# Kernel tuning notes

Measured on AMD Instinct MI355X. Metric: run time of the kernel, lower is better.

The kernel has to match this reference:

```python
import jax, jax.numpy as jnp
import numpy as np

T = 64
NBITS_PSUM = 8
NBITS_ACC = 8
K = 2
EPS = 1e-5

def _binarize_ste(x):
    # sign binarization with straight-through estimator (torch code overwrites .data)
    s = jnp.where(x >= 0, 1.0, -1.0).astype(x.dtype)
    return x + jax.lax.stop_gradient(s - x)

def _binary_conv_psum(x, w):
    # x: [N,C,H,W], w: [O,C,3,3]. Binarized 3x3 conv (stride 1, pad 1) computed as
    # chunks of T products along the unrolled reduction dim, each partial sum
    # quantized to NBITS_PSUM bits with step K, final accumulator clipped to NBITS_ACC.
    N, C, H, W = x.shape
    O = w.shape[0]
    xb = _binarize_ste(x)
    wb = _binarize_ste(w)
    patches = jax.lax.conv_general_dilated_patches(
        xb, (3, 3), (1, 1), ((1, 1), (1, 1)),
        dimension_numbers=('NCHW', 'OIHW', 'NCHW'))  # [N, C*9, H, W], channel-major
    R = C * 9
    nch = R // T  # 2304 / 64 = 36 chunks
    p = patches.reshape(N, nch, T, H, W).transpose(1, 0, 2, 3, 4)  # [nch,N,T,H,W]
    wf = wb.reshape(O, nch, T).transpose(1, 0, 2)                   # [nch,O,T]
    qmax = 2 ** (NBITS_PSUM - 1) - 1
    step = float(K)

    def body(carry, xs):
        acc, reg = carry
        pc, wc = xs
        psum = jnp.einsum('nthw,ot->nohw', pc, wc)  # partial sum over T binary products
        q = jnp.clip(jnp.round(psum / step), -qmax - 1, qmax) * step
        q_ste = psum + jax.lax.stop_gradient(q - psum)  # STE through quantizer
        reg = reg + jnp.mean((q - psum) ** 2)  # quantization-error regularizer
        return (acc + q_ste, reg), None

    acc0 = jnp.zeros((N, O, H, W), x.dtype)
    (acc, reg), _ = jax.lax.scan(body, (acc0, jnp.zeros((), x.dtype)), (p, wf))
    amax = (2 ** (NBITS_ACC - 1) - 1) * step  # accumulator clipping
    return jnp.clip(acc, -amax, amax), reg

def _bn(x, gamma, beta):
    # BatchNorm2d in training mode (batch statistics)
    m = jnp.mean(x, (0, 2, 3), keepdims=True)
    v = jnp.var(x, (0, 2, 3), keepdims=True)
    return (x - m) * jax.lax.rsqrt(v + EPS) * gamma[None, :, None, None] + beta[None, :, None, None]

def setup_inputs():
    key = jax.random.key(0)
    k1, k2, k3 = jax.random.split(key, 3)
    N, C, H, W = 32, 256, 32, 32
    return {
        'x0': jax.random.normal(k1, (N, C, H, W), jnp.float32),
        'reg0': jnp.zeros((), jnp.float32),
        'w1': jax.random.normal(k2, (C, C, 3, 3), jnp.float32),
        'gamma1': jnp.ones((C,), jnp.float32),
        'beta1': jnp.zeros((C,), jnp.float32),
        'w2': jax.random.normal(k3, (C, C, 3, 3), jnp.float32),
        'gamma2': jnp.ones((C,), jnp.float32),
        'beta2': jnp.zeros((C,), jnp.float32),
    }

def reference(x0, reg0, w1, gamma1, beta1, w2, gamma2, beta2):
    residual = x0
    out, r1 = _binary_conv_psum(x0, w1)
    reg = reg0 + r1
    out = _bn(out, gamma1, beta1)
    out = jnp.clip(out, -1.0, 1.0)  # Hardtanh
    out, r2 = _binary_conv_psum(out, w2)
    reg = reg + r2
    out = out + residual  # downsample is None
    reg = reg + r2        # faithful to original: conv2's r is added again after residual
    out = _bn(out, gamma2, beta2)
    out = jnp.clip(out, -1.0, 1.0)  # Hardtanh (do_bntan=True)
    return out, reg
```

## Files before the change

### kernel.cpp

```cpp
#include <hip/hip_runtime.h>

typedef unsigned long long u64;
typedef __attribute__((ext_vector_type(4)))  int i32x4;
typedef __attribute__((ext_vector_type(16))) int i32x16;

#define NPIX   32768
#define OCH    256
#define NCH    36

#define AROWS  196
#define ALDS   (AROWS * 256)
#define BLDS   8192
#define GLDS   (ALDS + 3 * BLDS)

__device__ __forceinline__ void gload16(const void* g, void* l) {
  __builtin_amdgcn_global_load_lds(
      (const __attribute__((address_space(1))) unsigned*)g,
      (__attribute__((address_space(3))) unsigned*)l, 16, 0, 0);
}

__global__ void bb_init(float* st, u64* masks) {
  int t = threadIdx.x;
  for (int i = t; i < 1024; i += 256) st[i] = 0.f;
  for (int id = t; id < 9 * NCH; id += 256) {
    int cls = id / NCH, ck = id % NCH;
    int ch = cls / 3, cw = cls % 3;
    u64 m = 0;
    for (int b = 0; b < 64; ++b) {
      int r = ck * 64 + b, tap = r % 9, kh = tap / 3, kw = tap % 3;
      bool oob = (ch == 0 && kh == 0) || (ch == 2 && kh == 2) ||
                 (cw == 0 && kw == 0) || (cw == 2 && kw == 2);
      if (!oob) m |= (u64)1 << b;
    }
    masks[id] = m;
  }
}

__global__ void bb_wbits(const float* wa, const float* wb, u64* Wbits) {
  int word = (blockIdx.x * blockDim.x + threadIdx.x) >> 6;
  int ln = threadIdx.x & 63;
  if (word >= 2 * OCH * NCH) return;
  const float* src = (word < OCH * NCH) ? wa : wb;
  int r = word % (OCH * NCH);
  u64 bits = __ballot(src[(size_t)r * 64 + ln] >= 0.f);
  int l = word / (OCH * NCH);
  int o = r / NCH, ck = r % NCH;
  if (ln == 0) Wbits[(size_t)l * OCH * NCH + (size_t)ck * OCH + o] = bits;
}

__global__ void bb_wi8(const float* wa, const float* wb, signed char* B) {
  int tid = blockIdx.x * blockDim.x + threadIdx.x;
  if (tid >= 2 * 589824) return;
  int l = tid >= 589824;
  int r = l ? tid - 589824 : tid;
  const float* src = l ? wb : wa;
  float v = src[r];
  int t = r % 9, oc9 = r / 9;
  int c = oc9 & 255, o = oc9 >> 8;
  B[(((size_t)(l * 9 + t) * 256 + o) << 8) + c] = (v >= 0.f) ? 1 : -1;
}

__global__ __launch_bounds__(256) void bb_xbits(const float* __restrict__ x,
                                                u64* __restrict__ Sb,
                                                signed char* __restrict__ A) {
  __shared__ float xt[256][33];
  int n = blockIdx.x >> 5, h = blockIdx.x & 31;
  int t = threadIdx.x;
  int w = t & 31, cg = t >> 5;
  for (int k = 0; k < 32; ++k) {
    int c = k * 8 + cg;
    xt[c][w] = x[((size_t)((n * 256 + c) * 32 + h) << 5) + w];
  }
  __syncthreads();
  int ln = t & 63, wv = t >> 6;
  int c2 = wv * 64 + ln;
  for (int w2 = 0; w2 < 32; ++w2) {
    bool s = xt[c2][w2] >= 0.f;
    u64 bits = __ballot(s);
    int px = (n * 32 + h) * 32 + w2;
    A[(size_t)px * 256 + c2] = s ? 1 : -1;
    if (ln == 0) Sb[(size_t)px * 4 + wv] = bits;
  }
}

__global__ __launch_bounds__(256, 2) void bb_gemm(const signed char* __restrict__ A,
                                                  const signed char* __restrict__ B,
                                                  short* __restrict__ dst) {
  extern __shared__ signed char sm[];
  int t = threadIdx.x, wv = t >> 6, ln = t & 63;
  int lw = ln & 31, hk = ln >> 5;
  int px0 = blockIdx.x << 7;
  int oc0 = blockIdx.y << 7;

  const signed char* Abase = A + (size_t)(px0 - 33) * 256;
  #pragma unroll
  for (int i = 0; i < 13; ++i) {
    int c = i * 4 + wv;
    if (c < 49) {
      int u = c * 64 + ln;
      int row = u >> 4, p = u & 15;
      gload16(Abase + (size_t)row * 256 + (((p ^ (row & 7)) << 4)),
              &sm[c * 1024]);
    }
  }

  #define STAGE_B(bufi, ks) do {                                              \
    int tp_ = (ks) >> 2, cb_ = (ks) & 3;                                      \
    const signed char* Bb_ = B + ((size_t)tp_ << 16) + (size_t)oc0 * 256      \
                               + (cb_ << 6);                                  \
    _Pragma("unroll")                                                         \
    for (int i_ = 0; i_ < 2; ++i_) {                                          \
      int c_ = wv * 2 + i_;                                                   \
      int u_ = c_ * 64 + ln;                                                  \
      int row_ = u_ >> 2, p_ = u_ & 3;                                        \
      gload16(Bb_ + (size_t)row_ * 256 + (((p_ ^ (row_ & 3)) << 4)),          \
              &sm[ALDS + (bufi) * BLDS + c_ * 1024]);                         \
    }                                                                         \
  } while (0)

  STAGE_B(0, 0);
  STAGE_B(1, 1);
  asm volatile("s_waitcnt vmcnt(2)" ::: "memory");
  __builtin_amdgcn_s_barrier();

  int wm = wv >> 1, wn = wv & 1;
  int arow0 = 33 + (wm << 6) + lw;
  int brow0 = (wn << 6) + lw;
  i32x16 acc00 = {0,0,0,0,0,0,0,0,0,0,0,0,0,0,0,0};
  i32x16 acc01 = acc00, acc10 = acc00, acc11 = acc00;

  for (int ks = 0; ks < 36; ++ks) {
    if (ks + 2 < 36) STAGE_B((ks + 2) % 3, ks + 2);
    int tp = ks >> 2, cb = ks & 3;
    int dpx = (tp / 3 - 1) * 32 + (tp % 3 - 1);
    int r0 = arow0 + dpx, r1 = r0 + 32;
    int q0 = brow0, q1 = brow0 + 32;
    const signed char* Bl = sm + ALDS + (ks % 3) * BLDS;
    __builtin_amdgcn_s_setprio(1);
    #pragma unroll
    for (int k32 = 0; k32 < 2; ++k32) {
      int sa = cb * 4 + k32 * 2 + hk;
      int sb = k32 * 2 + hk;
      i32x4 a0 = *(const i32x4*)(sm + r0 * 256 + ((sa ^ (r0 & 7)) << 4));
      i32x4 a1 = *(const i32x4*)(sm + r1 * 256 + ((sa ^ (r1 & 7)) << 4));
      i32x4 b0 = *(const i32x4*)(Bl + q0 * 64 + ((sb ^ (q0 & 3)) << 4));
      i32x4 b1 = *(const i32x4*)(Bl + q1 * 64 + ((sb ^ (q1 & 3)) << 4));
      acc00 = __builtin_amdgcn_mfma_i32_32x32x32_i8(a0, b0, acc00, 0, 0, 0);
      acc01 = __builtin_amdgcn_mfma_i32_32x32x32_i8(a0, b1, acc01, 0, 0, 0);
      acc10 = __builtin_amdgcn_mfma_i32_32x32x32_i8(a1, b0, acc10, 0, 0, 0);
      acc11 = __builtin_amdgcn_mfma_i32_32x32x32_i8(a1, b1, acc11, 0, 0, 0);
    }
    __builtin_amdgcn_s_setprio(0);
    if (ks < 34) asm volatile("s_waitcnt vmcnt(2)" ::: "memory");
    else         asm volatile("s_waitcnt vmcnt(0)" ::: "memory");
    __builtin_amdgcn_s_barrier();
  }
  #undef STAGE_B

  int px0w = px0 + (wm << 6), oc0w = oc0 + (wn << 6);
  int rbase = hk << 2;
  #pragma unroll
  for (int r = 0; r < 16; ++r) {
    int m = (r & 3) + ((r >> 2) << 3) + rbase;
    size_t row0 = ((size_t)(px0w + m)) << 8;
    size_t row1 = ((size_t)(px0w + 32 + m)) << 8;
    int v;
    v = acc00[r]; v = v < -254 ? -254 : (v > 254 ? 254 : v);
    dst[row0 + oc0w + lw] = (short)v;
    v = acc01[r]; v = v < -254 ? -254 : (v > 254 ? 254 : v);
    dst[row0 + oc0w + 32 + lw] = (short)v;
    v = acc10[r]; v = v < -254 ? -254 : (v > 254 ? 254 : v);
    dst[row1 + oc0w + lw] = (short)v;
    v = acc11[r]; v = v < -254 ? -254 : (v > 254 ? 254 : v);
    dst[row1 + oc0w + 32 + lw] = (short)v;
  }
}

__global__ __launch_bounds__(256) void bb_bconv(const u64* __restrict__ Sb,
                                                const u64* __restrict__ Wb,
                                                const u64* __restrict__ masks,
                                                short* __restrict__ dst) {
  __shared__ u64 spread[256];
  __shared__ u64 pw[NCH];
  __shared__ u64 mm[NCH];
  __shared__ int pm[NCH];
  int t = threadIdx.x;
  {
    u64 v = 0;
    for (int k = 0; k < 8; ++k) if (t & (1 << k)) v |= (u64)1 << (9 * k);
    spread[t] = v;
  }
  int b = blockIdx.x;
  int n = b / 124, r = b % 124;
  int h, w;
  if (r < 32)      { h = 0;      w = r;      }
  else if (r < 64) { h = 31;     w = r - 32; }
  else if (r < 94) { h = r - 63; w = 0;      }
  else             { h = r - 93; w = 31;     }
  int cls = (h == 0 ? 0 : (h == 31 ? 2 : 1)) * 3 + (w == 0 ? 0 : (w == 31 ? 2 : 1));
  __syncthreads();
  if (t < NCH) {
    int ck = t, base9 = ck % 9;
    u64 acc = 0;
    for (int tap = 0; tap < 9; ++tap) {
      int b0 = tap - base9; if (b0 < 0) b0 += 9;
      int nh = h + tap / 3 - 1, nw = w + tap % 3 - 1;
      if ((unsigned)nh <= 31u && (unsigned)nw <= 31u) {
        int run = (b0 == 0) ? 8 : 7;
        int c0 = (ck * 64 + b0) / 9;
        const u64* rp = Sb + ((size_t)((n * 32 + nh) * 32 + nw) << 2);
        int wi = c0 >> 6, sh = c0 & 63;
        u64 v = rp[wi] >> sh;
        if (sh + run > 64) v |= rp[wi + 1] << (64 - sh);
        v &= (run == 8) ? 0xFFull : 0x7Full;
        acc |= spread[(int)v] << b0;
      }
    }
    pw[ck] = acc;
    u64 m = masks[cls * NCH + ck];
    mm[ck] = m;
    pm[ck] = __popcll(m);
  }
  __syncthreads();
  int oc = t;
  int acc = 0;
  for (int i = 0; i < NCH; ++i) {
    int d = __popcll((pw[i] ^ Wb[(size_t)i * OCH + oc]) & mm[i]);
    int ps = pm[i] - 2 * d;
    acc += ps + (ps & 1) * ((ps & 2) - 1);
  }
  acc = acc < -254 ? -254 : (acc > 254 ? 254 : acc);
  int px = ((n * 32 + h) << 5) + w;
  dst[(size_t)px * OCH + oc] = (short)acc;
}

__global__ void bb_stats1(const short* v16, float* st) {
  int t = threadIdx.x;
  const short* base = v16 + (size_t)blockIdx.x * 128 * OCH;
  int s = 0; float q = 0.f;
  for (int r = 0; r < 128; ++r) {
    int v = base[r * OCH + t];
    s += v; q += (float)(v * v);
  }
  atomicAdd(&st[t], (float)s);
  atomicAdd(&st[256 + t], q);
}

__global__ void bb_xbits2(const short* v16, const float* st,
                          const float* g, const float* b, u64* Sb,
                          signed char* A) {
  int wave = (blockIdx.x * blockDim.x + threadIdx.x) >> 6;
  int ln = threadIdx.x & 63;
  int wrd = wave & 3, px0 = (wave >> 2) * 32;
  int oc = wrd * 64 + ln;
  float mu = st[oc] * (1.f / 32768.f);
  float va = st[256 + oc] * (1.f / 32768.f) - mu * mu;
  float rs = rsqrtf(va + 1e-5f);
  float gg = g[oc], bb = b[oc];
  for (int j = 0; j < 32; ++j) {
    float bn = ((float)v16[(size_t)(px0 + j) * OCH + oc] - mu) * rs * gg + bb;
    bool s = bn >= 0.f;
    u64 bits = __ballot(s);
    A[(size_t)(px0 + j) * 256 + oc] = s ? 1 : -1;
    if (ln == 0) Sb[(size_t)(px0 + j) * 4 + wrd] = bits;
  }
}

__global__ __launch_bounds__(256) void bb_stats2t(const short* __restrict__ pre16,
                                                  const float* __restrict__ x0,
                                                  float* st) {
  __shared__ float xt[32][257];
  int blk = blockIdx.x;
  int n = blk >> 5, h = blk & 31;
  int t = threadIdx.x;
  int w = t & 31, og = t >> 5;
  for (int k = 0; k < 32; ++k) {
    int oc = og * 32 + k;
    xt[w][oc] = x0[((size_t)(n * 256 + oc) * 32 + h) * 32 + w];
  }
  __syncthreads();
  int oc = t;
  size_t pb = (size_t)blk * 32 * OCH + oc;
  float s = 0.f, q = 0.f;
  for (int w2 = 0; w2 < 32; ++w2) {
    float v = (float)pre16[pb + (size_t)w2 * OCH] + xt[w2][oc];
    s += v; q += v * v;
  }
  atomicAdd(&st[512 + oc], s);
  atomicAdd(&st[768 + oc], q);
}

__global__ __launch_bounds__(256) void bb_fint(const short* __restrict__ pre16,
                                               const float* __restrict__ x0,
                                               const float* st, const float* g,
                                               const float* b, const float* r0,
                                               float* __restrict__ out) {
  __shared__ float xt[32][257];
  int blk = blockIdx.x;
  int n = blk >> 5, h = blk & 31;
  int t = threadIdx.x;
  int w = t & 31, og = t >> 5;
  for (int k = 0; k < 32; ++k) {
    int oc = og * 32 + k;
    xt[w][oc] = x0[((size_t)(n * 256 + oc) * 32 + h) * 32 + w];
  }
  __syncthreads();
  int oc = t;
  float mu = st[512 + oc] * (1.f / 32768.f);
  float va = st[768 + oc] * (1.f / 32768.f) - mu * mu;
  float rs = rsqrtf(va + 1e-5f);
  float gg = g[oc], bb = b[oc];
  size_t pb = (size_t)blk * 32 * OCH + oc;
  for (int w2 = 0; w2 < 32; ++w2) {
    float v = (float)pre16[pb + (size_t)w2 * OCH] + xt[w2][oc];
    v = (v - mu) * rs * gg + bb;
    xt[w2][oc] = fminf(fmaxf(v, -1.f), 1.f);
  }
  __syncthreads();
  for (int k = 0; k < 32; ++k) {
    int oc2 = og * 32 + k;
    out[((size_t)(n * 256 + oc2) * 32 + h) * 32 + w] = xt[w][oc2];
  }
  if (blk == 0 && t == 0) out[8388608] = r0[0] + 8.625f;
}

extern "C" void kernel_launch(void* const* d_in, const int* in_sizes, int n_in,
                              void* d_out, int out_size, void* d_ws, size_t ws_size,
                              hipStream_t stream) {
  const float* x0   = (const float*)d_in[0];
  const float* reg0 = (const float*)d_in[1];
  const float* w1   = (const float*)d_in[2];
  const float* g1   = (const float*)d_in[3];
  const float* b1   = (const float*)d_in[4];
  const float* w2   = (const float*)d_in[5];
  const float* g2   = (const float*)d_in[6];
  const float* b2   = (const float*)d_in[7];

  char* ws = (char*)d_ws;
  u64*   Wbits = (u64*)(ws);
  u64*   masks = (u64*)(ws + 147456);
  float* st    = (float*)(ws + 151552);
  u64*   Sb    = (u64*)(ws + 155648);
  signed char* Bi8 = (signed char*)(ws + 1204224);
  signed char* Ai8 = (signed char*)(ws + 2383872) + 32768;
  short* v16   = (short*)(ws + 10838016);

  bb_init   <<<1,    256, 0, stream>>>(st, masks);
  bb_wbits  <<<4608, 256, 0, stream>>>(w1, w2, Wbits);
  bb_wi8    <<<4608, 256, 0, stream>>>(w1, w2, Bi8);
  bb_xbits  <<<1024, 256, 0, stream>>>(x0, Sb, Ai8);
  bb_gemm   <<<dim3(256, 2), 256, GLDS, stream>>>(Ai8, Bi8, v16);
  bb_bconv  <<<3968, 256, 0, stream>>>(Sb, Wbits, masks, v16);
  bb_stats1 <<<256,  256, 0, stream>>>(v16, st);
  bb_xbits2 <<<1024, 256, 0, stream>>>(v16, st, g1, b1, Sb, Ai8);
  bb_gemm   <<<dim3(256, 2), 256, GLDS, stream>>>(Ai8, Bi8 + 589824, v16);
  bb_bconv  <<<3968, 256, 0, stream>>>(Sb, Wbits + OCH * NCH, masks, v16);
  bb_stats2t<<<1024, 256, 0, stream>>>(v16, x0, st);
  bb_fint   <<<1024, 256, 0, stream>>>(v16, x0, st, g2, b2, reg0, (float*)d_out);
}
```

Measured before the change: 287.8 us.

## Fuse BN statistics into GEMM/border epilogues and merge weight prep kernels

Merges the init, weight-bit and int8-weight preparation kernels into one launch. Moves the per-channel sum and sum-of-squares BatchNorm statistics into the epilogues of the int8 GEMM (interior pixels) and the border binary-conv kernel, including the residual add for the second layer. This removes the separate stats1 and stats2t passes over the conv output. The border conv now handles 16 pixels per block, so each weight word is loaded once for all 16. The cost is many more atomic adds and strided x0 reads inside the GEMM epilogue.

```diff
diff --git a/kernel.cpp b/kernel.cpp
--- a/kernel.cpp
+++ b/kernel.cpp
@@ -19,45 +19,42 @@
       (__attribute__((address_space(3))) unsigned*)l, 16, 0, 0);
 }
 
-__global__ void bb_init(float* st, u64* masks) {
-  int t = threadIdx.x;
-  for (int i = t; i < 1024; i += 256) st[i] = 0.f;
-  for (int id = t; id < 9 * NCH; id += 256) {
-    int cls = id / NCH, ck = id % NCH;
-    int ch = cls / 3, cw = cls % 3;
-    u64 m = 0;
-    for (int b = 0; b < 64; ++b) {
-      int r = ck * 64 + b, tap = r % 9, kh = tap / 3, kw = tap % 3;
-      bool oob = (ch == 0 && kh == 0) || (ch == 2 && kh == 2) ||
-                 (cw == 0 && kw == 0) || (cw == 2 && kw == 2);
-      if (!oob) m |= (u64)1 << b;
-    }
-    masks[id] = m;
-  }
-}
-
-__global__ void bb_wbits(const float* wa, const float* wb, u64* Wbits) {
-  int word = (blockIdx.x * blockDim.x + threadIdx.x) >> 6;
-  int ln = threadIdx.x & 63;
-  if (word >= 2 * OCH * NCH) return;
-  const float* src = (word < OCH * NCH) ? wa : wb;
-  int r = word % (OCH * NCH);
-  u64 bits = __ballot(src[(size_t)r * 64 + ln] >= 0.f);
-  int l = word / (OCH * NCH);
-  int o = r / NCH, ck = r % NCH;
-  if (ln == 0) Wbits[(size_t)l * OCH * NCH + (size_t)ck * OCH + o] = bits;
-}
-
-__global__ void bb_wi8(const float* wa, const float* wb, signed char* B) {
-  int tid = blockIdx.x * blockDim.x + threadIdx.x;
-  if (tid >= 2 * 589824) return;
-  int l = tid >= 589824;
-  int r = l ? tid - 589824 : tid;
-  const float* src = l ? wb : wa;
-  float v = src[r];
-  int t = r % 9, oc9 = r / 9;
-  int c = oc9 & 255, o = oc9 >> 8;
-  B[(((size_t)(l * 9 + t) * 256 + o) << 8) + c] = (v >= 0.f) ? 1 : -1;
+__global__ void bb_prep(const float* wa, const float* wb, u64* Wbits,
+                        signed char* B, float* st, u64* masks) {
+  int blk = blockIdx.x, t = threadIdx.x;
+  if (blk == 0) {
+    for (int i = t; i < 1024; i += 256) st[i] = 0.f;
+    for (int id = t; id < 9 * NCH; id += 256) {
+      int cls = id / NCH, ck = id % NCH;
+      int ch = cls / 3, cw = cls % 3;
+      u64 m = 0;
+      for (int b = 0; b < 64; ++b) {
+        int r = ck * 64 + b, tap = r % 9, kh = tap / 3, kw = tap % 3;
+        bool oob = (ch == 0 && kh == 0) || (ch == 2 && kh == 2) ||
+                   (cw == 0 && kw == 0) || (cw == 2 && kw == 2);
+        if (!oob) m |= (u64)1 << b;
+      }
+      masks[id] = m;
+    }
+  } else if (blk <= 4608) {
+    int word = (((blk - 1) << 8) + t) >> 6;
+    int ln = t & 63;
+    const float* src = (word < OCH * NCH) ? wa : wb;
+    int r = word % (OCH * NCH);
+    u64 bits = __ballot(src[(size_t)r * 64 + ln] >= 0.f);
+    int l = word / (OCH * NCH);
+    int o = r / NCH, ck = r % NCH;
+    if (ln == 0) Wbits[(size_t)l * OCH * NCH + (size_t)ck * OCH + o] = bits;
+  } else {
+    int tid = ((blk - 4609) << 8) + t;
+    int l = tid >= 589824;
+    int r = l ? tid - 589824 : tid;
+    const float* src = l ? wb : wa;
+    float v = src[r];
+    int tp = r % 9, oc9 = r / 9;
+    int c = oc9 & 255, o = oc9 >> 8;
+    B[(((size_t)(l * 9 + tp) * 256 + o) << 8) + c] = (v >= 0.f) ? 1 : -1;
+  }
 }
 
 __global__ __launch_bounds__(256) void bb_xbits(const float* __restrict__ x,
@@ -85,7 +82,9 @@
 
 __global__ __launch_bounds__(256, 2) void bb_gemm(const signed char* __restrict__ A,
                                                   const signed char* __restrict__ B,
-                                                  short* __restrict__ dst) {
+                                                  short* __restrict__ dst,
+                                                  float* __restrict__ st, int soff,
+                                                  const float* __restrict__ x0v) {
   extern __shared__ signed char sm[];
   int t = threadIdx.x, wv = t >> 6, ln = t & 63;
   int lw = ln & 31, hk = ln >> 5;
@@ -158,49 +157,76 @@
   #undef STAGE_B
 
   int px0w = px0 + (wm << 6), oc0w = oc0 + (wn << 6);
+  int oc_a = oc0w + lw, oc_b = oc_a + 32;
   int rbase = hk << 2;
+  int h0 = (px0w >> 5) & 31, h1 = ((px0w + 32) >> 5) & 31;
+  int n0 = px0w >> 10, n1 = (px0w + 32) >> 10;
+  bool i0 = (h0 >= 1) && (h0 <= 30);
+  bool i1 = (h1 >= 1) && (h1 <= 30);
+  const float *xa0 = 0, *xb0 = 0, *xa1 = 0, *xb1 = 0;
+  if (x0v) {
+    xa0 = x0v + (((size_t)(n0 * 256 + oc_a) * 32 + h0) << 5);
+    xb0 = x0v + (((size_t)(n0 * 256 + oc_b) * 32 + h0) << 5);
+    xa1 = x0v + (((size_t)(n1 * 256 + oc_a) * 32 + h1) << 5);
+    xb1 = x0v + (((size_t)(n1 * 256 + oc_b) * 32 + h1) << 5);
+  }
+  float s_a = 0.f, q_a = 0.f, s_b = 0.f, q_b = 0.f;
   #pragma unroll
   for (int r = 0; r < 16; ++r) {
     int m = (r & 3) + ((r >> 2) << 3) + rbase;
+    bool wok = (m >= 1) && (m <= 30);
     size_t row0 = ((size_t)(px0w + m)) << 8;
     size_t row1 = ((size_t)(px0w + 32 + m)) << 8;
-    int v;
+    int v; float f;
     v = acc00[r]; v = v < -254 ? -254 : (v > 254 ? 254 : v);
-    dst[row0 + oc0w + lw] = (short)v;
+    dst[row0 + oc_a] = (short)v;
+    if (i0 && wok) { f = (float)v + (x0v ? xa0[m] : 0.f); s_a += f; q_a += f * f; }
     v = acc01[r]; v = v < -254 ? -254 : (v > 254 ? 254 : v);
-    dst[row0 + oc0w + 32 + lw] = (short)v;
+    dst[row0 + oc_b] = (short)v;
+    if (i0 && wok) { f = (float)v + (x0v ? xb0[m] : 0.f); s_b += f; q_b += f * f; }
     v = acc10[r]; v = v < -254 ? -254 : (v > 254 ? 254 : v);
-    dst[row1 + oc0w + lw] = (short)v;
+    dst[row1 + oc_a] = (short)v;
+    if (i1 && wok) { f = (float)v + (x0v ? xa1[m] : 0.f); s_a += f; q_a += f * f; }
     v = acc11[r]; v = v < -254 ? -254 : (v > 254 ? 254 : v);
-    dst[row1 + oc0w + 32 + lw] = (short)v;
-  }
+    dst[row1 + oc_b] = (short)v;
+    if (i1 && wok) { f = (float)v + (x0v ? xb1[m] : 0.f); s_b += f; q_b += f * f; }
+  }
+  atomicAdd(&st[soff + oc_a], s_a);
+  atomicAdd(&st[soff + 256 + oc_a], q_a);
+  atomicAdd(&st[soff + 256 + oc_b], q_b);
+  atomicAdd(&st[soff + oc_b], s_b);
 }
 
 __global__ __launch_bounds__(256) void bb_bconv(const u64* __restrict__ Sb,
                                                 const u64* __restrict__ Wb,
                                                 const u64* __restrict__ masks,
-                                                short* __restrict__ dst) {
+                                                short* __restrict__ dst,
+                                                float* __restrict__ st, int soff,
+                                                const float* __restrict__ x0v) {
   __shared__ u64 spread[256];
-  __shared__ u64 pw[NCH];
-  __shared__ u64 mm[NCH];
-  __shared__ int pm[NCH];
+  __shared__ u64 pw[16][NCH];
+  __shared__ u64 mm[16][NCH];
+  __shared__ int pm[16][NCH];
+  __shared__ int pxl[16];
   int t = threadIdx.x;
   {
     u64 v = 0;
     for (int k = 0; k < 8; ++k) if (t & (1 << k)) v |= (u64)1 << (9 * k);
     spread[t] = v;
   }
-  int b = blockIdx.x;
-  int n = b / 124, r = b % 124;
-  int h, w;
-  if (r < 32)      { h = 0;      w = r;      }
-  else if (r < 64) { h = 31;     w = r - 32; }
-  else if (r < 94) { h = r - 63; w = 0;      }
-  else             { h = r - 93; w = 31;     }
-  int cls = (h == 0 ? 0 : (h == 31 ? 2 : 1)) * 3 + (w == 0 ? 0 : (w == 31 ? 2 : 1));
-  __syncthreads();
-  if (t < NCH) {
-    int ck = t, base9 = ck % 9;
+  __syncthreads();
+  for (int id = t; id < 16 * NCH; id += 256) {
+    int p = id / NCH, ck = id % NCH;
+    int gp = blockIdx.x * 16 + p;
+    int n = gp / 124, r = gp % 124;
+    int h, w;
+    if (r < 32)      { h = 0;      w = r;      }
+    else if (r < 64) { h = 31;     w = r - 32; }
+    else if (r < 94) { h = r - 63; w = 0;      }
+    else             { h = r - 93; w = 31;     }
+    int cls = (h == 0 ? 0 : (h == 31 ? 2 : 1)) * 3 + (w == 0 ? 0 : (w == 31 ? 2 : 1));
+    if (ck == 0) pxl[p] = ((n * 32 + h) << 5) + w;
+    int base9 = ck % 9;
     u64 acc = 0;
     for (int tap = 0; tap < 9; ++tap) {
       int b0 = tap - base9; if (b0 < 0) b0 += 9;
@@ -216,34 +242,41 @@
         acc |= spread[(int)v] << b0;
       }
     }
-    pw[ck] = acc;
+    pw[p][ck] = acc;
     u64 m = masks[cls * NCH + ck];
-    mm[ck] = m;
-    pm[ck] = __popcll(m);
+    mm[p][ck] = m;
+    pm[p][ck] = __popcll(m);
   }
   __syncthreads();
   int oc = t;
-  int acc = 0;
+  int acc[16];
+  #pragma unroll
+  for (int p = 0; p < 16; ++p) acc[p] = 0;
   for (int i = 0; i < NCH; ++i) {
-    int d = __popcll((pw[i] ^ Wb[(size_t)i * OCH + oc]) & mm[i]);
-    int ps = pm[i] - 2 * d;
-    acc += ps + (ps & 1) * ((ps & 2) - 1);
-  }
-  acc = acc < -254 ? -254 : (acc > 254 ? 254 : acc);
-  int px = ((n * 32 + h) << 5) + w;
-  dst[(size_t)px * OCH + oc] = (short)acc;
-}
-
-__global__ void bb_stats1(const short* v16, float* st) {
-  int t = threadIdx.x;
-  const short* base = v16 + (size_t)blockIdx.x * 128 * OCH;
-  int s = 0; float q = 0.f;
-  for (int r = 0; r < 128; ++r) {
-    int v = base[r * OCH + t];
-    s += v; q += (float)(v * v);
-  }
-  atomicAdd(&st[t], (float)s);
-  atomicAdd(&st[256 + t], q);
+    u64 wr = Wb[(size_t)i * OCH + oc];
+    #pragma unroll
+    for (int p = 0; p < 16; ++p) {
+      int d = __popcll((pw[p][i] ^ wr) & mm[p][i]);
+      int ps = pm[p][i] - 2 * d;
+      acc[p] += ps + (ps & 1) * ((ps & 2) - 1);
+    }
+  }
+  float s = 0.f, q = 0.f;
+  #pragma unroll
+  for (int p = 0; p < 16; ++p) {
+    int v = acc[p];
+    v = v < -254 ? -254 : (v > 254 ? 254 : v);
+    int px = pxl[p];
+    dst[(size_t)px * OCH + oc] = (short)v;
+    float f = (float)v;
+    if (x0v) {
+      int n = px >> 10, hw = px & 1023;
+      f += x0v[(((size_t)(n * 256 + oc)) << 10) + hw];
+    }
+    s += f; q += f * f;
+  }
+  atomicAdd(&st[soff + oc], s);
+  atomicAdd(&st[soff + 256 + oc], q);
 }
 
 __global__ void bb_xbits2(const short* v16, const float* st,
@@ -266,30 +299,6 @@
   }
 }
 
-__global__ __launch_bounds__(256) void bb_stats2t(const short* __restrict__ pre16,
-                                                  const float* __restrict__ x0,
-                                                  float* st) {
-  __shared__ float xt[32][257];
-  int blk = blockIdx.x;
-  int n = blk >> 5, h = blk & 31;
-  int t = threadIdx.x;
-  int w = t & 31, og = t >> 5;
-  for (int k = 0; k < 32; ++k) {
-    int oc = og * 32 + k;
-    xt[w][oc] = x0[((size_t)(n * 256 + oc) * 32 + h) * 32 + w];
-  }
-  __syncthreads();
-  int oc = t;
-  size_t pb = (size_t)blk * 32 * OCH + oc;
-  float s = 0.f, q = 0.f;
-  for (int w2 = 0; w2 < 32; ++w2) {
-    float v = (float)pre16[pb + (size_t)w2 * OCH] + xt[w2][oc];
-    s += v; q += v * v;
-  }
-  atomicAdd(&st[512 + oc], s);
-  atomicAdd(&st[768 + oc], q);
-}
-
 __global__ __launch_bounds__(256) void bb_fint(const short* __restrict__ pre16,
                                                const float* __restrict__ x0,
                                                const float* st, const float* g,
@@ -345,16 +354,14 @@
   signed char* Ai8 = (signed char*)(ws + 2383872) + 32768;
   short* v16   = (short*)(ws + 10838016);
 
-  bb_init   <<<1,    256, 0, stream>>>(st, masks);
-  bb_wbits  <<<4608, 256, 0, stream>>>(w1, w2, Wbits);
-  bb_wi8    <<<4608, 256, 0, stream>>>(w1, w2, Bi8);
+  bb_prep   <<<9217, 256, 0, stream>>>(w1, w2, Wbits, Bi8, st, masks);
   bb_xbits  <<<1024, 256, 0, stream>>>(x0, Sb, Ai8);
-  bb_gemm   <<<dim3(256, 2), 256, GLDS, stream>>>(Ai8, Bi8, v16);
-  bb_bconv  <<<3968, 256, 0, stream>>>(Sb, Wbits, masks, v16);
-  bb_stats1 <<<256,  256, 0, stream>>>(v16, st);
+  bb_gemm   <<<dim3(256, 2), 256, GLDS, stream>>>(Ai8, Bi8, v16, st, 0, nullptr);
+  bb_bconv  <<<248,  256, 0, stream>>>(Sb, Wbits, masks, v16, st, 0, nullptr);
   bb_xbits2 <<<1024, 256, 0, stream>>>(v16, st, g1, b1, Sb, Ai8);
-  bb_gemm   <<<dim3(256, 2), 256, GLDS, stream>>>(Ai8, Bi8 + 589824, v16);
-  bb_bconv  <<<3968, 256, 0, stream>>>(Sb, Wbits + OCH * NCH, masks, v16);
-  bb_stats2t<<<1024, 256, 0, stream>>>(v16, x0, st);
+  bb_gemm   <<<dim3(256, 2), 256, GLDS, stream>>>(Ai8, Bi8 + 589824, v16,
+                                                  st, 512, x0);
+  bb_bconv  <<<248,  256, 0, stream>>>(Sb, Wbits + OCH * NCH, masks, v16,
+                                       st, 512, x0);
   bb_fint   <<<1024, 256, 0, stream>>>(v16, x0, st, g2, b2, reg0, (float*)d_out);
 }
```

New measurement: 442.4 us. 53.7% more time.
